# Kernel tuning notes

Hardware: AMD Instinct MI355X
Metric: run time of the kernel (lower is better)

## Reference

```python
import jax, jax.numpy as jnp
import numpy as np

DEPTH = 3
B, D, O = 8192, 1024, 1024
HR = 32            # router hidden
HE = 2 * D         # expert hidden
N_NODES = 2 ** DEPTH - 1
N_LEAVES = 2 ** DEPTH


def setup_inputs() -> dict:
    key = jax.random.key(0)
    ks = jax.random.split(key, 9)
    x = jax.random.normal(ks[0], (B, D), dtype=jnp.float32)
    # decision-node router params (stacked over nodes)
    rW1 = jax.random.normal(ks[1], (N_NODES, D, HR), dtype=jnp.float32) * 0.05
    rb1 = jnp.zeros((N_NODES, HR), dtype=jnp.float32)
    rW2 = jax.random.normal(ks[2], (N_NODES, HR, 2), dtype=jnp.float32) * 0.05
    rb2 = jnp.zeros((N_NODES, 2), dtype=jnp.float32)
    # leaf-expert params (stacked over experts)
    eW1 = jax.random.normal(ks[3], (N_LEAVES, D, HE), dtype=jnp.float32) * 0.02
    eb1 = jnp.zeros((N_LEAVES, HE), dtype=jnp.float32)
    eW2 = jax.random.normal(ks[4], (N_LEAVES, HE, O), dtype=jnp.float32) * 0.02
    eb2 = jnp.zeros((N_LEAVES, O), dtype=jnp.float32)
    return {"x": x, "rW1": rW1, "rb1": rb1, "rW2": rW2, "rb2": rb2,
            "eW1": eW1, "eb1": eb1, "eW2": eW2, "eb2": eb2, "top_k": 4}


def _gelu(v):
    return jax.nn.gelu(v, approximate=False)  # torch nn.GELU default = exact erf


def _leaf_probs(x, rW1, rb1, rW2, rb2):
    # all decision nodes batched: [N, B, 2]
    h = _gelu(jnp.einsum('bd,ndh->nbh', x, rW1) + rb1[:, None, :])
    logits = jnp.einsum('nbh,nhc->nbc', h, rW2) + rb2[:, None, :]
    dec = jax.nn.softmax(logits, axis=-1)
    # BFS product of path probabilities, level by level (fixed small loop)
    probs = jnp.ones((x.shape[0], 1), dtype=x.dtype)
    start = 0
    for level in range(DEPTH):
        w = 2 ** level
        dl = dec[start:start + w].transpose(1, 0, 2)       # [B, w, 2]
        probs = (probs[:, :, None] * dl).reshape(x.shape[0], 2 * w)
        start += w
    return probs  # [B, N_LEAVES]


def reference(x, rW1, rb1, rW2, rb2, eW1, eb1, eW2, eb2, top_k):
    leaf_probs = _leaf_probs(x, rW1, rb1, rW2, rb2)
    if top_k is not None and top_k < N_LEAVES:
        vals, idx = jax.lax.top_k(leaf_probs, top_k)       # [B, k]
        sparse = jnp.zeros_like(leaf_probs)
        sparse = sparse.at[jnp.arange(leaf_probs.shape[0])[:, None], idx].set(vals)
        leaf_probs = sparse / (sparse.sum(axis=1, keepdims=True) + 1e-8)
    # all leaf experts, batched (dense weighted sum; skip heuristic is an approximation)
    h = _gelu(jnp.einsum('bd,edh->ebh', x, eW1) + eb1[:, None, :])   # [E, B, HE]
    out = jnp.einsum('ebh,eho->ebo', h, eW2) + eb2[:, None, :]        # [E, B, O]
    y = jnp.einsum('ebo,be->bo', out, leaf_probs)
    return (y, leaf_probs)
```

## Files before the change

kernel.cpp:

```cpp
#include <hip/hip_runtime.h>
#include <hip/hip_bf16.h>
#include <cstdint>

#define B_   8192
#define D_   1024
#define O_   1024
#define HE_  2048
#define NN_  7
#define NL_  8
#define HR_  32
#define RC_  224
#define K3_  3072
#define MTMAX_ 264

typedef __attribute__((ext_vector_type(2))) float f32x2;
typedef __attribute__((ext_vector_type(4))) float f32x4;
typedef __attribute__((ext_vector_type(8))) short bf16x8;
typedef __attribute__((ext_vector_type(4))) unsigned short u16x4;
typedef unsigned short u16;
typedef unsigned int u32;

__device__ __forceinline__ u16 f2bf(float f) {
  __hip_bfloat16 h = __float2bfloat16(f);
  return *reinterpret_cast<u16*>(&h);
}
__device__ __forceinline__ float bf2f(u16 u) {
  u32 v = ((u32)u) << 16;
  return *reinterpret_cast<float*>(&v);
}
__device__ __forceinline__ float gelu_exact(float v) {
  return 0.5f * v * (1.0f + erff(v * 0.7071067811865475f));
}
__device__ __forceinline__ void gload16(const void* g, void* l) {
  __builtin_amdgcn_global_load_lds(
      (const __attribute__((address_space(1))) void*)(uintptr_t)g,
      (__attribute__((address_space(3))) void*)(uintptr_t)l,
      16, 0, 0);
}
#define WAITVM(n) asm volatile("s_waitcnt vmcnt(" #n ")" ::: "memory")
#define WAITLGKM0 do { \
  asm volatile("s_waitcnt lgkmcnt(0)" ::: "memory"); \
  __builtin_amdgcn_sched_barrier(0); } while (0)

__device__ __forceinline__ bool expert_of_tile(
    const int* __restrict__ counts, int mt,
    int& e, int& cnt, long& m0, long& hbase) {
  int tot = 0; e = -1; cnt = 0; int tofe = 0;
#pragma unroll
  for (int f = 0; f < NL_; f++) {
    int c = counts[f];
    int tl = (c + 127) >> 7;
    bool in = (e < 0) && (mt < tot + tl);
    if (in) { e = f; tofe = tot; cnt = c; }
    tot += tl;
  }
  if (e < 0) return false;
  m0 = (long)(mt - tofe) * 128;
  hbase = (long)tofe * 128;
  return true;
}

__global__ __launch_bounds__(256) void prep_kernel(
    const float* __restrict__ x, const float* __restrict__ rW1,
    const float* __restrict__ eW1, const float* __restrict__ eW2,
    u16* __restrict__ Xbs, u16* __restrict__ Wr3,
    u16* __restrict__ W1t, u16* __restrict__ W2t) {
  __shared__ __attribute__((aligned(16))) float tile[64][65];
  int bid = blockIdx.x;
  int t = threadIdx.x;
  if (bid < 8192) {
    const float* in; u16* out; int C, ldo; long in_e, out_e;
    int bx, by, bz;
    if (bid < 4096) {
      in = eW1; out = W1t; C = HE_; ldo = D_;
      in_e = (long)D_ * HE_; out_e = (long)HE_ * D_;
      bx = bid & 31; by = (bid >> 5) & 15; bz = bid >> 9;
    } else {
      int b = bid - 4096;
      in = eW2; out = W2t; C = O_; ldo = HE_;
      in_e = (long)HE_ * O_; out_e = (long)O_ * HE_;
      bx = b & 15; by = (b >> 4) & 31; bz = b >> 9;
    }
    const float* in_p = in + bz * in_e;
    u16* out_p = out + bz * out_e;
    int r0 = by * 64, c0 = bx * 64;
    int cc = t & 63, rbase = t >> 6;
#pragma unroll
    for (int i = 0; i < 16; i++) {
      int rr = rbase + i * 4;
      tile[rr][cc] = in_p[(long)(r0 + rr) * C + c0 + cc];
    }
    __syncthreads();
    int r2 = (t & 31) * 2, cj = t >> 5;
#pragma unroll
    for (int i = 0; i < 8; i++) {
      int c = cj * 8 + i;
      u32 u = (u32)f2bf(tile[r2][c]) | ((u32)f2bf(tile[r2 + 1][c]) << 16);
      *reinterpret_cast<u32*>(out_p + (long)(c0 + c) * ldo + r0 + r2) = u;
    }
  } else if (bid < 16384) {
    size_t i = ((size_t)(bid - 8192) * 256 + t) * 4;
    size_t row = i >> 10;
    int col = (int)(i & 1023);
    f32x4 f = *reinterpret_cast<const f32x4*>(x + i);
    u16x4 hi, lo;
#pragma unroll
    for (int j = 0; j < 4; j++) {
      hi[j] = f2bf(f[j]);
      lo[j] = f2bf(f[j] - bf2f(hi[j]));
    }
    u16* base = Xbs + row * 2048 + col;
    *reinterpret_cast<u16x4*>(base)        = hi;
    *reinterpret_cast<u16x4*>(base + 1024) = lo;
  } else {
    size_t i = ((size_t)(bid - 16384) * 256 + t) * 4;
    int c = (int)(i / K3_), k = (int)(i % K3_);
    int j = k >> 10, kk = k & 1023;
    u16x4 o;
    if (c < RC_) {
      int node = c >> 5, h = c & 31;
      const float* src = rW1 + ((size_t)node * 1024 + kk) * HR_ + h;
#pragma unroll
      for (int q = 0; q < 4; q++) {
        float f = src[q * HR_];
        u16 hi = f2bf(f);
        o[q] = (j == 1) ? f2bf(f - bf2f(hi)) : hi;
      }
    } else {
      o[0] = 0; o[1] = 0; o[2] = 0; o[3] = 0;
    }
    *reinterpret_cast<u16x4*>(Wr3 + i) = o;
  }
}

__global__ __launch_bounds__(256, 2) void router_gemm_kernel(
    const u16* __restrict__ Xbs, const u16* __restrict__ Bm,
    float* __restrict__ H1p) {
  __shared__ __attribute__((aligned(16))) u16 lA[128 * 32];
  __shared__ __attribute__((aligned(16))) u16 lB[128 * 32];
  int tid = threadIdx.x;
  int gid = blockIdx.x;
  int cpx = gridDim.x >> 3;
  gid = (gid & 7) * cpx + (gid >> 3);
  int s = gid >> 7;
  int rem = gid & 127;
  int band = rem >> 4, inb = rem & 15;
  long m0 = (long)(band * 8 + (inb & 7)) * 128;
  long n0 = (long)(inb >> 3) * 128;
  int wid = tid >> 6, lane = tid & 63;
  int wm = wid >> 1, wn = wid & 1;
  f32x4 acc[4][4];
#pragma unroll
  for (int m = 0; m < 4; m++)
#pragma unroll
    for (int n = 0; n < 4; n++) acc[m][n] = (f32x4){0.f, 0.f, 0.f, 0.f};
  int lr = lane & 15, lk = (lane >> 4) * 8;
  int srow = tid >> 2, soff = (tid & 3) * 8;
  const u16* Bb = Bm + n0 * K3_;
  int kbeg = s * 768, kend = kbeg + 768;
  for (int k0 = kbeg; k0 < kend; k0 += 32) {
    int ca = (k0 < 1024) ? k0 : k0 - 1024;
    gload16(Xbs + (m0 + srow) * 2048 + ca + soff, &lA[tid * 8]);
    gload16(Xbs + (m0 + 64 + srow) * 2048 + ca + soff, &lA[(256 + tid) * 8]);
    gload16(Bb + (long)srow * K3_ + k0 + soff, &lB[tid * 8]);
    gload16(Bb + (long)(64 + srow) * K3_ + k0 + soff, &lB[(256 + tid) * 8]);
    __syncthreads();
    bf16x8 af[4], bfr[4];
#pragma unroll
    for (int m = 0; m < 4; m++)
      af[m] = *reinterpret_cast<const bf16x8*>(&lA[(wm * 64 + m * 16 + lr) * 32 + lk]);
#pragma unroll
    for (int n = 0; n < 4; n++)
      bfr[n] = *reinterpret_cast<const bf16x8*>(&lB[(wn * 64 + n * 16 + lr) * 32 + lk]);
#pragma unroll
    for (int m = 0; m < 4; m++)
#pragma unroll
      for (int n = 0; n < 4; n++)
        acc[m][n] = __builtin_amdgcn_mfma_f32_16x16x32_bf16(af[m], bfr[n], acc[m][n], 0, 0, 0);
    __syncthreads();
  }
  int lq = lane >> 4;
#pragma unroll
  for (int m = 0; m < 4; m++)
#pragma unroll
    for (int n = 0; n < 4; n++)
#pragma unroll
      for (int j = 0; j < 4; j++) {
        long row = m0 + wm * 64 + m * 16 + lq * 4 + j;
        long col = n0 + wn * 64 + n * 16 + lr;
        if (col < RC_)
          H1p[((long)s * B_ + row) * RC_ + col] = acc[m][n][j];
      }
}

__global__ __launch_bounds__(256) void router_logits_kernel(
    const float* __restrict__ H1p, const float* __restrict__ rb1,
    const float* __restrict__ rW2, const float* __restrict__ rb2,
    const int* __restrict__ topk_ptr, float* __restrict__ P) {
  int b = blockIdx.x * 256 + threadIdx.x;
  float dec[NN_][2];
#pragma unroll
  for (int n = 0; n < NN_; n++) {
    float l0 = rb2[n * 2], l1 = rb2[n * 2 + 1];
#pragma unroll
    for (int r4 = 0; r4 < HR_; r4 += 4) {
      int c = n * HR_ + r4;
      f32x4 hs = *reinterpret_cast<const f32x4*>(&H1p[((long)0 * B_ + b) * RC_ + c]);
#pragma unroll
      for (int s = 1; s < 4; s++)
        hs += *reinterpret_cast<const f32x4*>(&H1p[((long)s * B_ + b) * RC_ + c]);
      f32x4 bv = *reinterpret_cast<const f32x4*>(rb1 + c);
#pragma unroll
      for (int j = 0; j < 4; j++) {
        float hv = gelu_exact(hs[j] + bv[j]);
        l0 += hv * rW2[(c + j) * 2];
        l1 += hv * rW2[(c + j) * 2 + 1];
      }
    }
    float mx = fmaxf(l0, l1);
    float e0 = expf(l0 - mx), e1 = expf(l1 - mx);
    float sm = e0 + e1;
    dec[n][0] = e0 / sm; dec[n][1] = e1 / sm;
  }
  float v[NL_];
#pragma unroll
  for (int L = 0; L < NL_; L++)
    v[L] = dec[0][L >> 2] * dec[1 + (L >> 2)][(L >> 1) & 1] * dec[3 + (L >> 1)][L & 1];
  int tk = *topk_ptr;
  float p[NL_];
  if (tk < NL_) {
    float s = 0.f;
    bool keep[NL_];
#pragma unroll
    for (int e = 0; e < NL_; e++) {
      int rank = 0;
#pragma unroll
      for (int j = 0; j < NL_; j++)
        rank += ((v[j] > v[e]) || (v[j] == v[e] && j < e)) ? 1 : 0;
      keep[e] = rank < tk;
      if (keep[e]) s += v[e];
    }
    float inv = 1.f / (s + 1e-8f);
#pragma unroll
    for (int e = 0; e < NL_; e++) p[e] = keep[e] ? v[e] * inv : 0.f;
  } else {
#pragma unroll
    for (int e = 0; e < NL_; e++) p[e] = v[e];
  }
#pragma unroll
  for (int e = 0; e < NL_; e++) P[(long)b * NL_ + e] = p[e];
}

__global__ __launch_bounds__(256) void tail_kernel(
    const float* __restrict__ P, const float* __restrict__ eb2,
    float* __restrict__ y, int* __restrict__ idx, int* __restrict__ counts) {
  __shared__ int wsum[4];
  __shared__ int sbase;
  int t = threadIdx.x;
  if (blockIdx.x < 8192) {
    size_t i = ((size_t)blockIdx.x * 256 + t) * 4;
    size_t row = i >> 10;
    int col = (int)(i & 1023);
    f32x4 s = (f32x4){0.f, 0.f, 0.f, 0.f};
#pragma unroll
    for (int e = 0; e < NL_; e++) {
      float pe = P[row * NL_ + e];
      f32x4 w = *reinterpret_cast<const f32x4*>(eb2 + (size_t)e * O_ + col);
      s += w * pe;
    }
    *reinterpret_cast<f32x4*>(y + i) = s;
  } else {
    int e = blockIdx.x - 8192;
    int wave = t >> 6, lane = t & 63;
    if (t == 0) sbase = 0;
    __syncthreads();
    for (int c0 = 0; c0 < B_; c0 += 256) {
      int r = c0 + t;
      bool f = P[(long)r * NL_ + e] > 0.f;
      unsigned long long mask = __ballot(f);
      int intra = __popcll(mask & ((1ULL << lane) - 1ULL));
      if (lane == 0) wsum[wave] = __popcll(mask);
      __syncthreads();
      int wpre = 0;
#pragma unroll
      for (int w = 0; w < 4; w++) wpre += (w < wave) ? wsum[w] : 0;
      int tot = wsum[0] + wsum[1] + wsum[2] + wsum[3];
      if (f) idx[(long)e * B_ + sbase + wpre + intra] = r;
      __syncthreads();
      if (t == 0) sbase += tot;
      __syncthreads();
    }
    if (t == 0) counts[e] = sbase;
  }
}

__global__ __launch_bounds__(256, 2) void gemme1_kernel(
    const u16* __restrict__ Xbs, const u16* __restrict__ W1t,
    const float* __restrict__ eb1, const float* __restrict__ P,
    u16* __restrict__ Hall, const int* __restrict__ idx,
    const int* __restrict__ counts) {
  __shared__ __attribute__((aligned(16))) u16 lA[128 * 64];
  __shared__ __attribute__((aligned(16))) u16 lB[128 * 64];
  int tid = threadIdx.x;
  int gid = blockIdx.x;
  int cpx = gridDim.x >> 3;
  gid = (gid & 7) * cpx + (gid >> 3);
  int mt = gid >> 4, nt = gid & 15;
  int e, cnt; long m0, hbase;
  if (!expert_of_tile(counts, mt, e, cnt, m0, hbase)) return;
  long n0 = (long)nt * 128;
  const int* idxe = idx + (long)e * B_;
  int wid = tid >> 6, lane = tid & 63;
  int wm = wid >> 1, wn = wid & 1;
  f32x4 acc[4][4];
#pragma unroll
  for (int m = 0; m < 4; m++)
#pragma unroll
    for (int n = 0; n < 4; n++) acc[m][n] = (f32x4){0.f, 0.f, 0.f, 0.f};
  int lr = lane & 15, lkg = lane >> 4;
  const u16* gA[4]; const u16* gB[4]; int lds_o[4];
  const u16* Bb = W1t + ((size_t)e * HE_ + n0) * D_;
#pragma unroll
  for (int i = 0; i < 4; i++) {
    int sidx = tid + i * 256;
    int r = sidx >> 3, j = sidx & 7;
    int so = ((j ^ (r & 7)) << 3);
    int gi = (m0 + r < cnt) ? idxe[m0 + r] : 0;
    gA[i] = Xbs + (long)gi * 2048 + so;
    gB[i] = Bb + (long)r * D_ + so;
    lds_o[i] = sidx * 8;
  }
  int foA[4][2], foB[4][2];
#pragma unroll
  for (int m = 0; m < 4; m++) {
    int r = wm * 64 + m * 16 + lr;
#pragma unroll
    for (int kk = 0; kk < 2; kk++)
      foA[m][kk] = r * 128 + ((((kk * 4 + lkg) ^ (r & 7))) << 4);
  }
#pragma unroll
  for (int n = 0; n < 4; n++) {
    int r = wn * 64 + n * 16 + lr;
#pragma unroll
    for (int kk = 0; kk < 2; kk++)
      foB[n][kk] = r * 128 + ((((kk * 4 + lkg) ^ (r & 7))) << 4);
  }
  const char* pa = (const char*)lA;
  const char* pb = (const char*)lB;
  for (int k0 = 0; k0 < D_; k0 += 64) {
#pragma unroll
    for (int i = 0; i < 4; i++) gload16(gA[i] + k0, &lA[lds_o[i]]);
#pragma unroll
    for (int i = 0; i < 4; i++) gload16(gB[i] + k0, &lB[lds_o[i]]);
    __syncthreads();
    bf16x8 af[4][2], bfr[4][2];
#pragma unroll
    for (int m = 0; m < 4; m++) {
      af[m][0] = *reinterpret_cast<const bf16x8*>(pa + foA[m][0]);
      af[m][1] = *reinterpret_cast<const bf16x8*>(pa + foA[m][1]);
    }
#pragma unroll
    for (int n = 0; n < 4; n++) {
      bfr[n][0] = *reinterpret_cast<const bf16x8*>(pb + foB[n][0]);
      bfr[n][1] = *reinterpret_cast<const bf16x8*>(pb + foB[n][1]);
    }
#pragma unroll
    for (int m = 0; m < 4; m++)
#pragma unroll
      for (int n = 0; n < 4; n++) {
        acc[m][n] = __builtin_amdgcn_mfma_f32_16x16x32_bf16(af[m][0], bfr[n][0], acc[m][n], 0, 0, 0);
        acc[m][n] = __builtin_amdgcn_mfma_f32_16x16x32_bf16(af[m][1], bfr[n][1], acc[m][n], 0, 0, 0);
      }
    __syncthreads();
  }
  int lq = lane >> 4;
#pragma unroll
  for (int m = 0; m < 4; m++) {
#pragma unroll
    for (int j = 0; j < 4; j++) {
      long lrow = m0 + wm * 64 + m * 16 + lq * 4 + j;
      if (lrow >= cnt) continue;
      int orow = idxe[lrow];
      float pw = P[(long)orow * NL_ + e];
#pragma unroll
      for (int n = 0; n < 4; n++) {
        long col = n0 + wn * 64 + n * 16 + lr;
        float g = gelu_exact(acc[m][n][j] + eb1[(size_t)e * HE_ + col]);
        Hall[(hbase + lrow) * HE_ + col] = f2bf(g * pw);
      }
    }
  }
}

__global__ __launch_bounds__(256, 2) void gemme2_kernel(
    const u16* __restrict__ Hall, const u16* __restrict__ W2t,
    float* __restrict__ y, const int* __restrict__ idx,
    const int* __restrict__ counts) {
  __shared__ __attribute__((aligned(16))) u16 lA[2][128 * 64];
  __shared__ __attribute__((aligned(16))) u16 lB[2][128 * 64];
  int tid = threadIdx.x;
  int gid = blockIdx.x;
  int cpx = gridDim.x >> 3;
  gid = (gid & 7) * cpx + (gid >> 3);
  int mt = gid >> 3, nt = gid & 7;
  int e, cnt; long m0, hbase;
  if (!expert_of_tile(counts, mt, e, cnt, m0, hbase)) return;
  long n0 = (long)nt * 128;
  const int* idxe = idx + (long)e * B_;
  int wid = tid >> 6, lane = tid & 63;
  int wm = wid >> 1, wn = wid & 1;
  f32x4 acc[4][4];
#pragma unroll
  for (int m = 0; m < 4; m++)
#pragma unroll
    for (int n = 0; n < 4; n++) acc[m][n] = (f32x4){0.f, 0.f, 0.f, 0.f};
  int lr = lane & 15, lkg = lane >> 4;
  const u16* Ab = Hall + (hbase + m0) * HE_;
  const u16* Bb = W2t + ((size_t)e * O_ + n0) * HE_;
  const u16* gA[4]; const u16* gB[4]; int lds_o[4];
#pragma unroll
  for (int i = 0; i < 4; i++) {
    int sidx = tid + i * 256;
    int r = sidx >> 3, j = sidx & 7;
    int so = ((j ^ (r & 7)) << 3);
    gA[i] = Ab + (long)r * HE_ + so;
    gB[i] = Bb + (long)r * HE_ + so;
    lds_o[i] = sidx * 8;
  }
  int foA[4][2], foB[4][2];
#pragma unroll
  for (int m = 0; m < 4; m++) {
    int r = wm * 64 + m * 16 + lr;
#pragma unroll
    for (int kk = 0; kk < 2; kk++)
      foA[m][kk] = r * 128 + ((((kk * 4 + lkg) ^ (r & 7))) << 4);
  }
#pragma unroll
  for (int n = 0; n < 4; n++) {
    int r = wn * 64 + n * 16 + lr;
#pragma unroll
    for (int kk = 0; kk < 2; kk++)
      foB[n][kk] = r * 128 + ((((kk * 4 + lkg) ^ (r & 7))) << 4);
  }
#define STAGE2(buf, k0) do { _Pragma("unroll") \
  for (int i_ = 0; i_ < 4; i_++) gload16(gA[i_] + (k0), &lA[buf][lds_o[i_]]); \
  _Pragma("unroll") \
  for (int i_ = 0; i_ < 4; i_++) gload16(gB[i_] + (k0), &lB[buf][lds_o[i_]]); \
  } while (0)
  STAGE2(0, 0);
  int cur = 0;
  constexpr int NT = HE_ / 64;
  for (int t = 0; t < NT; ++t) {
    if (t + 1 < NT) {
      STAGE2(cur ^ 1, (t + 1) * 64);
      WAITVM(8);
    } else {
      WAITVM(0);
    }
    __builtin_amdgcn_s_barrier();
    __builtin_amdgcn_sched_barrier(0);
    const char* pa = (const char*)lA[cur];
    const char* pb = (const char*)lB[cur];
    bf16x8 af[4][2], bfr[4][2];
#pragma unroll
    for (int m = 0; m < 4; m++) {
      af[m][0] = *reinterpret_cast<const bf16x8*>(pa + foA[m][0]);
      af[m][1] = *reinterpret_cast<const bf16x8*>(pa + foA[m][1]);
    }
#pragma unroll
    for (int n = 0; n < 4; n++) {
      bfr[n][0] = *reinterpret_cast<const bf16x8*>(pb + foB[n][0]);
      bfr[n][1] = *reinterpret_cast<const bf16x8*>(pb + foB[n][1]);
    }
    WAITLGKM0;
    __builtin_amdgcn_s_setprio(1);
#pragma unroll
    for (int m = 0; m < 4; m++)
#pragma unroll
      for (int n = 0; n < 4; n++) {
        acc[m][n] = __builtin_amdgcn_mfma_f32_16x16x32_bf16(af[m][0], bfr[n][0], acc[m][n], 0, 0, 0);
        acc[m][n] = __builtin_amdgcn_mfma_f32_16x16x32_bf16(af[m][1], bfr[n][1], acc[m][n], 0, 0, 0);
      }
    __builtin_amdgcn_s_setprio(0);
    __builtin_amdgcn_s_barrier();
    __builtin_amdgcn_sched_barrier(0);
    cur ^= 1;
  }
#undef STAGE2
  int lq = lane >> 4;
#pragma unroll
  for (int m = 0; m < 4; m++) {
#pragma unroll
    for (int j = 0; j < 4; j++) {
      long lrow = m0 + wm * 64 + m * 16 + lq * 4 + j;
      if (lrow >= cnt) continue;
      long orow = idxe[lrow];
#pragma unroll
      for (int n = 0; n < 4; n++) {
        long col = n0 + wn * 64 + n * 16 + lr;
        unsafeAtomicAdd(&y[orow * O_ + col], acc[m][n][j]);
      }
    }
  }
}

extern "C" void kernel_launch(void* const* d_in, const int* in_sizes, int n_in,
                              void* d_out, int out_size, void* d_ws, size_t ws_size,
                              hipStream_t stream) {
  (void)in_sizes; (void)n_in; (void)out_size; (void)ws_size;
  const float* x   = (const float*)d_in[0];
  const float* rW1 = (const float*)d_in[1];
  const float* rb1 = (const float*)d_in[2];
  const float* rW2 = (const float*)d_in[3];
  const float* rb2 = (const float*)d_in[4];
  const float* eW1 = (const float*)d_in[5];
  const float* eb1 = (const float*)d_in[6];
  const float* eW2 = (const float*)d_in[7];
  const float* eb2 = (const float*)d_in[8];
  const int*  topk = (const int*)d_in[9];
  float* y = (float*)d_out;
  float* P = y + (size_t)B_ * O_;

  char* ws = (char*)d_ws;
  u16*  Xbs = (u16*)ws;
  u16*  W1t = (u16*)(ws + 33554432);
  u16*  W2t = (u16*)(ws + 67108864);
  int*  idx    = (int*)(ws + 100663296);
  int*  counts = (int*)(ws + 100925440);
  char* hreg   = ws + 100925952;
  u16*  Hall = (u16*)hreg;
  u16*  Wr3  = (u16*)hreg;
  float* H1p = (float*)(hreg + 2097152);

  prep_kernel<<<17152, 256, 0, stream>>>(x, rW1, eW1, eW2, Xbs, Wr3, W1t, W2t);
  router_gemm_kernel<<<512, 256, 0, stream>>>(Xbs, Wr3, H1p);
  router_logits_kernel<<<B_ / 256, 256, 0, stream>>>(H1p, rb1, rW2, rb2, topk, P);
  tail_kernel<<<8200, 256, 0, stream>>>(P, eb2, y, idx, counts);

  gemme1_kernel<<<MTMAX_ * 16, 256, 0, stream>>>(
      Xbs, W1t, eb1, P, Hall, idx, counts);
  gemme2_kernel<<<MTMAX_ * 8, 256, 0, stream>>>(
      Hall, W2t, y, idx, counts);
}
```

Before: 622.7 us.

## Widen expert-GEMM1 tile to 128x256 with split B fragment loads and setprio

The first expert GEMM now uses a 128x256 output tile instead of 128x128, halving the grid and doubling the per-wave accumulator set to 4x8 MFMA tiles. The B operand tile grows to 256 rows in LDS and is consumed in two halves, each followed by an LDS wait and a raised wave priority around the MFMA burst. The aim is to reuse each A (gathered X rows) tile across twice as many output columns, cutting global and LDS traffic for A per FLOP. In exchange it raises register and LDS use (48KB shared), which may reduce occupancy and leaves fewer blocks to fill the GPU.

```diff
diff --git a/kernel.cpp b/kernel.cpp
--- a/kernel.cpp
+++ b/kernel.cpp
@@ -300,26 +300,25 @@
     u16* __restrict__ Hall, const int* __restrict__ idx,
     const int* __restrict__ counts) {
   __shared__ __attribute__((aligned(16))) u16 lA[128 * 64];
-  __shared__ __attribute__((aligned(16))) u16 lB[128 * 64];
+  __shared__ __attribute__((aligned(16))) u16 lB[256 * 64];
   int tid = threadIdx.x;
   int gid = blockIdx.x;
   int cpx = gridDim.x >> 3;
   gid = (gid & 7) * cpx + (gid >> 3);
-  int mt = gid >> 4, nt = gid & 15;
+  int mt = gid >> 3, nt = gid & 7;
   int e, cnt; long m0, hbase;
   if (!expert_of_tile(counts, mt, e, cnt, m0, hbase)) return;
-  long n0 = (long)nt * 128;
+  long n0 = (long)nt * 256;
   const int* idxe = idx + (long)e * B_;
   int wid = tid >> 6, lane = tid & 63;
   int wm = wid >> 1, wn = wid & 1;
-  f32x4 acc[4][4];
+  f32x4 acc[4][8];
 #pragma unroll
   for (int m = 0; m < 4; m++)
 #pragma unroll
-    for (int n = 0; n < 4; n++) acc[m][n] = (f32x4){0.f, 0.f, 0.f, 0.f};
+    for (int n = 0; n < 8; n++) acc[m][n] = (f32x4){0.f, 0.f, 0.f, 0.f};
   int lr = lane & 15, lkg = lane >> 4;
-  const u16* gA[4]; const u16* gB[4]; int lds_o[4];
-  const u16* Bb = W1t + ((size_t)e * HE_ + n0) * D_;
+  const u16* gA[4]; int ldsA[4];
 #pragma unroll
   for (int i = 0; i < 4; i++) {
     int sidx = tid + i * 256;
@@ -327,8 +326,17 @@
     int so = ((j ^ (r & 7)) << 3);
     int gi = (m0 + r < cnt) ? idxe[m0 + r] : 0;
     gA[i] = Xbs + (long)gi * 2048 + so;
-    gB[i] = Bb + (long)r * D_ + so;
-    lds_o[i] = sidx * 8;
+    ldsA[i] = sidx * 8;
+  }
+  const u16* Bb = W1t + ((size_t)e * HE_ + n0) * D_;
+  int gBo[8]; int ldsB[8];
+#pragma unroll
+  for (int i = 0; i < 8; i++) {
+    int sidx = tid + i * 256;
+    int r = sidx >> 3, j = sidx & 7;
+    int so = ((j ^ (r & 7)) << 3);
+    gBo[i] = r * D_ + so;
+    ldsB[i] = sidx * 8;
   }
   int foA[4][2], foB[4][2];
 #pragma unroll
@@ -340,7 +348,7 @@
   }
 #pragma unroll
   for (int n = 0; n < 4; n++) {
-    int r = wn * 64 + n * 16 + lr;
+    int r = wn * 128 + n * 16 + lr;
 #pragma unroll
     for (int kk = 0; kk < 2; kk++)
       foB[n][kk] = r * 128 + ((((kk * 4 + lkg) ^ (r & 7))) << 4);
@@ -349,9 +357,9 @@
   const char* pb = (const char*)lB;
   for (int k0 = 0; k0 < D_; k0 += 64) {
 #pragma unroll
-    for (int i = 0; i < 4; i++) gload16(gA[i] + k0, &lA[lds_o[i]]);
-#pragma unroll
-    for (int i = 0; i < 4; i++) gload16(gB[i] + k0, &lB[lds_o[i]]);
+    for (int i = 0; i < 4; i++) gload16(gA[i] + k0, &lA[ldsA[i]]);
+#pragma unroll
+    for (int i = 0; i < 8; i++) gload16(Bb + gBo[i] + k0, &lB[ldsB[i]]);
     __syncthreads();
     bf16x8 af[4][2], bfr[4][2];
 #pragma unroll
@@ -364,6 +372,8 @@
       bfr[n][0] = *reinterpret_cast<const bf16x8*>(pb + foB[n][0]);
       bfr[n][1] = *reinterpret_cast<const bf16x8*>(pb + foB[n][1]);
     }
+    WAITLGKM0;
+    __builtin_amdgcn_s_setprio(1);
 #pragma unroll
     for (int m = 0; m < 4; m++)
 #pragma unroll
@@ -371,6 +381,22 @@
         acc[m][n] = __builtin_amdgcn_mfma_f32_16x16x32_bf16(af[m][0], bfr[n][0], acc[m][n], 0, 0, 0);
         acc[m][n] = __builtin_amdgcn_mfma_f32_16x16x32_bf16(af[m][1], bfr[n][1], acc[m][n], 0, 0, 0);
       }
+    __builtin_amdgcn_s_setprio(0);
+#pragma unroll
+    for (int n = 0; n < 4; n++) {
+      bfr[n][0] = *reinterpret_cast<const bf16x8*>(pb + foB[n][0] + 8192);
+      bfr[n][1] = *reinterpret_cast<const bf16x8*>(pb + foB[n][1] + 8192);
+    }
+    WAITLGKM0;
+    __builtin_amdgcn_s_setprio(1);
+#pragma unroll
+    for (int m = 0; m < 4; m++)
+#pragma unroll
+      for (int n = 0; n < 4; n++) {
+        acc[m][n + 4] = __builtin_amdgcn_mfma_f32_16x16x32_bf16(af[m][0], bfr[n][0], acc[m][n + 4], 0, 0, 0);
+        acc[m][n + 4] = __builtin_amdgcn_mfma_f32_16x16x32_bf16(af[m][1], bfr[n][1], acc[m][n + 4], 0, 0, 0);
+      }
+    __builtin_amdgcn_s_setprio(0);
     __syncthreads();
   }
   int lq = lane >> 4;
@@ -383,8 +409,8 @@
       int orow = idxe[lrow];
       float pw = P[(long)orow * NL_ + e];
 #pragma unroll
-      for (int n = 0; n < 4; n++) {
-        long col = n0 + wn * 64 + n * 16 + lr;
+      for (int n = 0; n < 8; n++) {
+        long col = n0 + wn * 128 + (n & 3) * 16 + (n >> 2) * 64 + lr;
         float g = gelu_exact(acc[m][n][j] + eb1[(size_t)e * HE_ + col]);
         Hall[(hbase + lrow) * HE_ + col] = f2bf(g * pw);
       }
@@ -537,7 +563,7 @@
   router_logits_kernel<<<B_ / 256, 256, 0, stream>>>(H1p, rb1, rW2, rb2, topk, P);
   tail_kernel<<<8200, 256, 0, stream>>>(P, eb2, y, idx, counts);
 
-  gemme1_kernel<<<MTMAX_ * 16, 256, 0, stream>>>(
+  gemme1_kernel<<<MTMAX_ * 8, 256, 0, stream>>>(
       Xbs, W1t, eb1, P, Hall, idx, counts);
   gemme2_kernel<<<MTMAX_ * 8, 256, 0, stream>>>(
       Hall, W2t, y, idx, counts);
```

Measured after the change: 665.4 us. 6.9% more time.

## Double-buffer expert GEMM1 LDS tiles with BK=32 and async prefetch

Applied to the files above, without the earlier changes.

Replaces the single-buffered BK=64 LDS loop in the first expert GEMM with a two-stage ping-pong buffer at BK=32. The loads for the next tile are issued before the current tile's MFMAs, using a partial vmcnt wait, raw s_barrier and scheduling barriers. MFMA priority is also raised around the math block. The goal is to hide global-to-LDS latency behind compute, at the cost of twice as many iterations and barriers with less work in each.

```diff
diff --git a/kernel.cpp b/kernel.cpp
--- a/kernel.cpp
+++ b/kernel.cpp
@@ -299,8 +299,8 @@
     const float* __restrict__ eb1, const float* __restrict__ P,
     u16* __restrict__ Hall, const int* __restrict__ idx,
     const int* __restrict__ counts) {
-  __shared__ __attribute__((aligned(16))) u16 lA[128 * 64];
-  __shared__ __attribute__((aligned(16))) u16 lB[128 * 64];
+  __shared__ __attribute__((aligned(16))) u16 lA[2][128 * 32];
+  __shared__ __attribute__((aligned(16))) u16 lB[2][128 * 32];
   int tid = threadIdx.x;
   int gid = blockIdx.x;
   int cpx = gridDim.x >> 3;
@@ -318,61 +318,68 @@
 #pragma unroll
     for (int n = 0; n < 4; n++) acc[m][n] = (f32x4){0.f, 0.f, 0.f, 0.f};
   int lr = lane & 15, lkg = lane >> 4;
-  const u16* gA[4]; const u16* gB[4]; int lds_o[4];
+  const u16* gA[2]; const u16* gB[2]; int lds_o[2];
   const u16* Bb = W1t + ((size_t)e * HE_ + n0) * D_;
 #pragma unroll
-  for (int i = 0; i < 4; i++) {
+  for (int i = 0; i < 2; i++) {
     int sidx = tid + i * 256;
-    int r = sidx >> 3, j = sidx & 7;
-    int so = ((j ^ (r & 7)) << 3);
+    int r = sidx >> 2, j = sidx & 3;
+    int so = ((j ^ ((r >> 1) & 3)) << 3);
     int gi = (m0 + r < cnt) ? idxe[m0 + r] : 0;
     gA[i] = Xbs + (long)gi * 2048 + so;
     gB[i] = Bb + (long)r * D_ + so;
     lds_o[i] = sidx * 8;
   }
-  int foA[4][2], foB[4][2];
+  int foA[4], foB[4];
 #pragma unroll
   for (int m = 0; m < 4; m++) {
     int r = wm * 64 + m * 16 + lr;
-#pragma unroll
-    for (int kk = 0; kk < 2; kk++)
-      foA[m][kk] = r * 128 + ((((kk * 4 + lkg) ^ (r & 7))) << 4);
+    foA[m] = r * 64 + (((lkg ^ ((r >> 1) & 3))) << 4);
   }
 #pragma unroll
   for (int n = 0; n < 4; n++) {
     int r = wn * 64 + n * 16 + lr;
-#pragma unroll
-    for (int kk = 0; kk < 2; kk++)
-      foB[n][kk] = r * 128 + ((((kk * 4 + lkg) ^ (r & 7))) << 4);
-  }
-  const char* pa = (const char*)lA;
-  const char* pb = (const char*)lB;
-  for (int k0 = 0; k0 < D_; k0 += 64) {
-#pragma unroll
-    for (int i = 0; i < 4; i++) gload16(gA[i] + k0, &lA[lds_o[i]]);
-#pragma unroll
-    for (int i = 0; i < 4; i++) gload16(gB[i] + k0, &lB[lds_o[i]]);
-    __syncthreads();
-    bf16x8 af[4][2], bfr[4][2];
-#pragma unroll
-    for (int m = 0; m < 4; m++) {
-      af[m][0] = *reinterpret_cast<const bf16x8*>(pa + foA[m][0]);
-      af[m][1] = *reinterpret_cast<const bf16x8*>(pa + foA[m][1]);
-    }
-#pragma unroll
-    for (int n = 0; n < 4; n++) {
-      bfr[n][0] = *reinterpret_cast<const bf16x8*>(pb + foB[n][0]);
-      bfr[n][1] = *reinterpret_cast<const bf16x8*>(pb + foB[n][1]);
-    }
+    foB[n] = r * 64 + (((lkg ^ ((r >> 1) & 3))) << 4);
+  }
+#define STAGE1(buf, k0) do { _Pragma("unroll") \
+  for (int i_ = 0; i_ < 2; i_++) gload16(gA[i_] + (k0), &lA[buf][lds_o[i_]]); \
+  _Pragma("unroll") \
+  for (int i_ = 0; i_ < 2; i_++) gload16(gB[i_] + (k0), &lB[buf][lds_o[i_]]); \
+  } while (0)
+  STAGE1(0, 0);
+  int cur = 0;
+  constexpr int NT = D_ / 32;
+  for (int t = 0; t < NT; ++t) {
+    if (t + 1 < NT) {
+      STAGE1(cur ^ 1, (t + 1) * 32);
+      WAITVM(4);
+    } else {
+      WAITVM(0);
+    }
+    __builtin_amdgcn_s_barrier();
+    __builtin_amdgcn_sched_barrier(0);
+    const char* pa = (const char*)lA[cur];
+    const char* pb = (const char*)lB[cur];
+    bf16x8 af[4], bfr[4];
 #pragma unroll
     for (int m = 0; m < 4; m++)
-#pragma unroll
-      for (int n = 0; n < 4; n++) {
-        acc[m][n] = __builtin_amdgcn_mfma_f32_16x16x32_bf16(af[m][0], bfr[n][0], acc[m][n], 0, 0, 0);
-        acc[m][n] = __builtin_amdgcn_mfma_f32_16x16x32_bf16(af[m][1], bfr[n][1], acc[m][n], 0, 0, 0);
-      }
-    __syncthreads();
-  }
+      af[m] = *reinterpret_cast<const bf16x8*>(pa + foA[m]);
+#pragma unroll
+    for (int n = 0; n < 4; n++)
+      bfr[n] = *reinterpret_cast<const bf16x8*>(pb + foB[n]);
+    WAITLGKM0;
+    __builtin_amdgcn_s_setprio(1);
+#pragma unroll
+    for (int m = 0; m < 4; m++)
+#pragma unroll
+      for (int n = 0; n < 4; n++)
+        acc[m][n] = __builtin_amdgcn_mfma_f32_16x16x32_bf16(af[m], bfr[n], acc[m][n], 0, 0, 0);
+    __builtin_amdgcn_s_setprio(0);
+    __builtin_amdgcn_s_barrier();
+    __builtin_amdgcn_sched_barrier(0);
+    cur ^= 1;
+  }
+#undef STAGE1
   int lq = lane >> 4;
 #pragma unroll
   for (int m = 0; m < 4; m++) {
```

After: 619.0 us (median of 2 runs). No clear change (-0.6%).
